# Performance work log

Hardware: AMD Instinct MI355X
Metric: run time of the kernel (lower is better)

Reference implementation:

```python
import jax, jax.numpy as jnp
import numpy as np

N = 100000; S = 8; V = 10000; DE = 64; DH = 64; H = DH + 6; T = 2; E = 250000
MAXP = 10; SZ = 64; OUT = MAXP * SZ; NPLAIN = 6; NAR = 2


def setup_inputs() -> dict:
    key = jax.random.key(0)
    ks = jax.random.split(key, 20)
    rn = lambda k, sh, s=0.1: jax.random.normal(k, sh, jnp.float32) * s
    return {
        "tokens": jax.random.randint(ks[0], (N, S), 0, V, jnp.int32),
        "type_idx": jax.random.randint(ks[1], (N,), 0, 6, jnp.int32),
        "edge_src": jax.random.randint(ks[2], (T, E), 0, N, jnp.int32),
        "edge_dst": jax.random.randint(ks[3], (T, E), 0, N, jnp.int32),
        "map_entry_idx": 123,
        "embed": rn(ks[4], (V, DE), 0.3),
        "Wi_map": rn(ks[5], (3 * DH, DE)), "Wh_map": rn(ks[6], (3 * DH, DH)),
        "bi_map": jnp.zeros((3 * DH,), jnp.float32), "bh_map": jnp.zeros((3 * DH,), jnp.float32),
        "Wi_mem": rn(ks[7], (3 * DH, DE)), "Wh_mem": rn(ks[8], (3 * DH, DH)),
        "bi_mem": jnp.zeros((3 * DH,), jnp.float32), "bh_mem": jnp.zeros((3 * DH,), jnp.float32),
        "Wm_plain": rn(ks[9], (NPLAIN, T, H, H)), "bm_plain": jnp.zeros((NPLAIN, T, H), jnp.float32),
        "Wu_plain": rn(ks[10], (NPLAIN, 2 * H, H)), "bu_plain": jnp.zeros((NPLAIN, H), jnp.float32),
        "Wm_ar": rn(ks[11], (NAR, T, 2 * H, 2 * H)), "bm_ar": jnp.zeros((NAR, T, 2 * H), jnp.float32),
        "Wu_ar": rn(ks[12], (NAR, 4 * H, H)), "bu_ar": jnp.zeros((NAR, H), jnp.float32),
        "W1": rn(ks[13], (H, H)), "b1": jnp.zeros((H,), jnp.float32),
        "W2": rn(ks[14], (H, OUT)), "b2": jnp.zeros((OUT,), jnp.float32),
    }


def _gru_last(x_seq, Wi, Wh, bi, bh):
    # x_seq: [S, N, DE] -> last hidden [N, DH] (torch nn.GRU cell math)
    def step(h, x):
        gi = x @ Wi.T + bi
        gh = h @ Wh.T + bh
        ir, iz, inn = jnp.split(gi, 3, axis=-1)
        hr, hz, hn = jnp.split(gh, 3, axis=-1)
        r = jax.nn.sigmoid(ir + hr)
        z = jax.nn.sigmoid(iz + hz)
        n = jnp.tanh(inn + r * hn)
        return (1.0 - z) * n + z * h, None
    h0 = jnp.zeros((x_seq.shape[1], Wh.shape[1]), x_seq.dtype)
    h, _ = jax.lax.scan(step, h0, x_seq)
    return h


def _mp(h, src, dst, Wm, bm, Wu, bu, msg_act, dense_act):
    # per-edge-type linear message on sender state, scatter-max aggregation, dense update
    m = jnp.einsum('ted,tdm->tem', h[src], Wm) + bm[:, None, :]  # [T, E, M]
    if msg_act is not None:
        m = msg_act(m)
    agg = jax.ops.segment_max(m.reshape(-1, m.shape[-1]), dst.reshape(-1), num_segments=h.shape[0])
    agg = jnp.where(jnp.isneginf(agg), 0.0, agg)  # nodes with no incoming edges -> 0
    u = jnp.concatenate([h, agg], axis=-1) @ Wu + bu
    return dense_act(u) if dense_act is not None else u


def _forward(tokens, type_idx, edge_src, edge_dst, map_entry_idx, embed,
             Wi_map, Wh_map, bi_map, bh_map, Wi_mem, Wh_mem, bi_mem, bh_mem,
             Wm_plain, bm_plain, Wu_plain, bu_plain, Wm_ar, bm_ar, Wu_ar, bu_ar,
             W1, b1, W2, b2):
    x_seq = embed[tokens].transpose(1, 0, 2)  # [S, N, DE]
    h_map = _gru_last(x_seq, Wi_map, Wh_map, bi_map, bh_map)
    h_mem = _gru_last(x_seq, Wi_mem, Wh_mem, bi_mem, bh_mem)
    is_map = (type_idx == 0)[:, None]
    is_mem = (type_idx == 5)[:, None]
    node_h = jnp.where(is_map, h_map, jnp.where(is_mem, h_mem, 0.0))
    h = jnp.concatenate([jax.nn.one_hot(type_idx, 6, dtype=node_h.dtype), node_h], axis=-1)  # [N, H]
    li = 0
    for blk in range(2):  # two concat-residual blocks from create_mlp_mp_layers
        saved = h
        for _ in range(3):  # plain MLP MP layers: no msg/dense activation
            h = _mp(h, edge_src, edge_dst, Wm_plain[li], bm_plain[li], Wu_plain[li], bu_plain[li], None, None)
            li += 1
        h = jnp.concatenate([saved, h], axis=-1)  # ConcatResidualLayer -> [N, 2H]
        h = _mp(h, edge_src, edge_dst, Wm_ar[blk], bm_ar[blk], Wu_ar[blk], bu_ar[blk], jax.nn.gelu, jnp.tanh)
    x = h[map_entry_idx]            # select map entry node
    x = jax.nn.relu(x @ W1 + b1)    # trans_layers[0]
    return x @ W2 + b2


def reference(tokens, type_idx, edge_src, edge_dst, map_entry_idx, embed,
              Wi_map, Wh_map, bi_map, bh_map, Wi_mem, Wh_mem, bi_mem, bh_mem,
              Wm_plain, bm_plain, Wu_plain, bu_plain, Wm_ar, bm_ar, Wu_ar, bu_ar,
              W1, b1, W2, b2):
    return _forward(tokens, type_idx, edge_src, edge_dst, map_entry_idx, embed,
                    Wi_map, Wh_map, bi_map, bh_map, Wi_mem, Wh_mem, bi_mem, bh_mem,
                    Wm_plain, bm_plain, Wu_plain, bu_plain, Wm_ar, bm_ar, Wu_ar, bu_ar,
                    W1, b1, W2, b2)
```

## Files before the change

### kernel.cpp

```cpp
#include <hip/hip_runtime.h>
#include <math.h>

#define CAPT 20480
#define R2   (2*CAPT)
#define GLD  136
#define GRR  32

typedef __attribute__((ext_vector_type(8))) short short8;
typedef __attribute__((ext_vector_type(4))) float f32x4;

__device__ __forceinline__ float fexp2_(float x){ return __builtin_amdgcn_exp2f(x); }
__device__ __forceinline__ float frcp_(float x){ return __builtin_amdgcn_rcpf(x); }
__device__ __forceinline__ float ftanh_(float x){
  float t = fexp2_(2.885390082f * x);
  return __builtin_fmaf(-2.f, frcp_(1.f + t), 1.f);
}
__device__ __forceinline__ float fsig_(float x){
  return frcp_(1.f + fexp2_(-1.442695041f * x));
}
__device__ __forceinline__ float fgelu_(float x){
  float x2 = x*x;
  float u  = x * __builtin_fmaf(x2, 0.044715f, 1.0f);
  float e  = fexp2_(u * -2.30220818f);
  return x * frcp_(1.f + e);
}
__device__ __forceinline__ unsigned short f2bf(float x){
  unsigned int u = __float_as_uint(x);
  return (unsigned short)((u + 0x7FFFu + ((u>>16)&1u)) >> 16);
}
__device__ __forceinline__ float bf2f(unsigned short v){
  return __uint_as_float(((unsigned int)v) << 16);
}
__device__ __forceinline__ unsigned int cvt_pk_bf16(float a, float b){
  unsigned int r;
  asm("v_cvt_pk_bf16_f32 %0, %1, %2" : "=v"(r) : "v"(a), "v"(b));
  return r;
}

__global__ void k_prepB(const float* __restrict__ Wm_plain, const float* __restrict__ Wu_plain,
                        const float* __restrict__ Wm_ar, const float* __restrict__ Wu_ar,
                        const float* __restrict__ Wi_map, const float* __restrict__ Wh_map,
                        const float* __restrict__ Wi_mem, const float* __restrict__ Wh_mem,
                        unsigned short* __restrict__ BtArena){
  int id = blockIdx.y;
  int Kp, elems, off;
  if (id < 6){ Kp=96;  elems=15360; off=id*15360; }
  else if (id < 12){ Kp=160; elems=12800; off=92160+(id-6)*12800; }
  else if (id < 14){ Kp=160; elems=51200; off=168960+(id-12)*51200; }
  else if (id < 16){ Kp=320; elems=25600; off=271360+(id-14)*25600; }
  else { Kp=128; elems=32768; off=322560+(id-16)*32768; }
  for (int g = blockIdx.x*256 + threadIdx.x; g < elems; g += 8*256){
    int c = g / Kp, k = g - c*Kp;
    float val = 0.f;
    if (id < 6){
      int li = id; int t = (c >= 80); int cc = c - t*80;
      if (cc < 70 && k < 70) val = Wm_plain[((li*2+t)*70 + k)*70 + cc];
    } else if (id < 12){
      int li = id-6;
      int kk = (k < 70) ? k : ((k >= 80 && k < 150) ? 70 + (k-80) : -1);
      if (c < 70 && kk >= 0) val = Wu_plain[(li*140 + kk)*70 + c];
    } else if (id < 14){
      int blk = id-12; int t = (c >= 160); int cc = c - t*160;
      int kk = (k < 70) ? k : ((k >= 80 && k < 150) ? 70 + (k-80) : -1);
      if (cc < 140 && kk >= 0) val = Wm_ar[(((blk*2+t)*140) + kk)*140 + cc];
    } else if (id < 16){
      int blk = id-14;
      int kk = (k < 70) ? k : ((k >= 80 && k < 150) ? 70 + (k-80)
               : ((k >= 160 && k < 300) ? 140 + (k-160) : -1));
      if (c < 70 && kk >= 0) val = Wu_ar[(blk*280 + kk)*70 + c];
    } else {
      int typ = id-16;
      const float* Wi = typ ? Wi_mem : Wi_map;
      const float* Wh = typ ? Wh_mem : Wh_map;
      if (c < 192) val = (k < 64) ? Wi[c*64 + k] : Wh[c*64 + (k-64)];
      else { int cc = c-192; val = (k >= 64) ? Wh[(128+cc)*64 + (k-64)] : 0.f; }
    }
    BtArena[off + g] = f2bf(val);
  }
}

__global__ void k_prepBias(const float* __restrict__ bm_plain, const float* __restrict__ bu_plain,
                           const float* __restrict__ bm_ar, const float* __restrict__ bu_ar,
                           const float* __restrict__ bi_map, const float* __restrict__ bh_map,
                           const float* __restrict__ bi_mem, const float* __restrict__ bh_mem,
                           float* __restrict__ biasA){
  for (int g = threadIdx.x; g < 2752; g += 256){
    float val = 0.f;
    if (g < 960){ int li=g/160, c=g%160; int t=(c>=80); int cc=c-t*80;
      if (cc<70) val = bm_plain[(li*2+t)*70 + cc]; }
    else if (g < 1440){ int u=g-960; int li=u/80, c=u%80; if (c<70) val = bu_plain[li*70+c]; }
    else if (g < 2080){ int u=g-1440; int blk=u/320, c=u%320; int t=(c>=160); int cc=c-t*160;
      if (cc<140) val = bm_ar[(blk*2+t)*140 + cc]; }
    else if (g < 2240){ int u=g-2080; int blk=u/80, c=u%80; if (c<70) val = bu_ar[blk*70+c]; }
    else { int u=g-2240; int typ=u/256, c=u%256;
      const float* bi = typ ? bi_mem : bi_map; const float* bh = typ ? bh_mem : bh_map;
      val = (c < 192) ? (bi[c]+bh[c]) : bh[128 + (c-192)]; }
    biasA[g] = val;
  }
}

__global__ void k_prepEmb(const float* __restrict__ embed, unsigned short* __restrict__ embB,
                          int total){
  int g = blockIdx.x*256 + threadIdx.x;
  if (g < total) embB[g] = f2bf(embed[g]);
}

__global__ void k_init_h(const int* __restrict__ type_idx, unsigned short* __restrict__ h, int N){
  int g = blockIdx.x*256 + threadIdx.x;
  if (g >= N*80) return;
  int n = g / 80, c = g - n*80;
  h[g] = (c < 6 && type_idx[n] == c) ? (unsigned short)0x3F80 : (unsigned short)0;
}

__global__ void k_compact(const int* __restrict__ type_idx, int* __restrict__ idxcat,
                          int* __restrict__ cnt, int N){
  int n = blockIdx.x*256 + threadIdx.x;
  if (n >= N) return;
  int t = type_idx[n];
  if (t == 0){ int p = atomicAdd(&cnt[0],1); if (p < CAPT) idxcat[p] = n; }
  else if (t == 5){ int p = atomicAdd(&cnt[1],1); if (p < CAPT) idxcat[CAPT+p] = n; }
}

__global__ void k_count(const int* __restrict__ edst, int* __restrict__ deg, int TE){
  int i = blockIdx.x*256 + threadIdx.x;
  if (i < TE) atomicAdd(&deg[edst[i]], 1);
}
__global__ void k_scan1(const int* __restrict__ deg, int* __restrict__ off,
                        int* __restrict__ bsum, int N){
  __shared__ int sh[256];
  int t = threadIdx.x; int base = blockIdx.x*2048;
  int v[8]; int s = 0;
  for (int i=0;i<8;i++){
    int g = base + t*8 + i;
    int x = (g<N)? (((deg[g]+3)>>2)<<2) : 0;
    v[i]=x; s+=x;
  }
  sh[t]=s; __syncthreads();
  for (int o=1;o<256;o<<=1){ int x = (t>=o)? sh[t-o]:0; __syncthreads(); sh[t]+=x; __syncthreads(); }
  if (t==255) bsum[blockIdx.x] = sh[255];
  int run = sh[t]-s;
  for (int i=0;i<8;i++){ int g = base + t*8 + i; if (g<N) off[g]=run; run+=v[i]; }
}
__global__ void k_scan2(int* bsum, int nb){
  if (threadIdx.x==0 && blockIdx.x==0){
    int run=0;
    for(int b=0;b<nb;b++){ int x=bsum[b]; bsum[b]=run; run+=x; }
    bsum[nb]=run;
  }
}
__global__ void k_scan3(int* __restrict__ off, const int* __restrict__ bsum, int N, int nb){
  int g = blockIdx.x*256+threadIdx.x;
  if (g < N) off[g] += bsum[g>>11];
  if (g == 0) off[N] = bsum[nb];
}
__global__ void k_fill(const int* __restrict__ esrc, const int* __restrict__ edst,
                       const int* __restrict__ off, int* __restrict__ cur,
                       int* __restrict__ edata, int TE, int E){
  int i = blockIdx.x*256 + threadIdx.x;
  if (i >= TE) return;
  int d = edst[i];
  int pos = off[d] + atomicAdd(&cur[d], 1);
  edata[pos] = (esrc[i] << 1) | (i >= E ? 1 : 0);
}
__global__ void k_pad(const int* __restrict__ off, const int* __restrict__ cur,
                      int* __restrict__ edata, int N){
  int n = blockIdx.x*256 + threadIdx.x;
  if (n >= N) return;
  int d = cur[n];
  if (d == 0) return;
  int d4 = ((d+3)>>2)<<2;
  int base = off[n];
  int first = edata[base];
  for (int i = d; i < d4; i++) edata[base+i] = first;
}

__global__ __launch_bounds__(256) void kgru(
    const int* __restrict__ idxcat, const int* __restrict__ tokens,
    const unsigned short* __restrict__ embB,
    const unsigned short* __restrict__ Bt, const unsigned short* __restrict__ Bt2,
    const float* __restrict__ bias, const float* __restrict__ bias2,
    unsigned short* __restrict__ hOut)
{
  __shared__ __align__(16) unsigned short As[2][GRR*GLD];
  __shared__ int tokS[GRR*8];
  __shared__ int idxS[GRR];
  int rb = blockIdx.y * CAPT + blockIdx.x * GRR;
  if (idxcat[rb] < 0) return;
  int t = threadIdx.x;
  int lane = t & 63, m = lane & 15, q = lane >> 4, w = t >> 6;
  const unsigned short* Bsel = blockIdx.y ? Bt2 : Bt;
  const float* bsel = blockIdx.y ? bias2 : bias;
  short8 breg[4][4]; float bv[4];
  #pragma unroll
  for (int j=0;j<4;j++){
    int col = (w + 4*j)*16 + m;
    bv[j] = bsel[col];
    #pragma unroll
    for (int kt=0;kt<4;kt++)
      breg[j][kt] = *(const short8*)&Bsel[(size_t)col*128 + kt*32 + q*8];
  }
  if (t < GRR) idxS[t] = idxcat[rb + t];
  if (t < GRR*8){
    int nd = idxcat[rb + (t>>3)]; if (nd < 0) nd = 0;
    tokS[t] = tokens[nd*8 + (t & 7)];
  }
  __syncthreads();
  if (t < GRR*8){
    int row = t >> 3, ch = t & 7;
    *(uint4*)&As[0][row*GLD + ch*8] = *(const uint4*)&embB[(size_t)tokS[row*8]*64 + ch*8];
  }
  for (int j = t; j < GRR*32; j += 256){
    int row = j >> 5, k2 = (j & 31)*2;
    *(unsigned int*)&As[0][row*GLD + 64 + k2] = 0;
  }
  __syncthreads();
  unsigned short hreg[2][4];
  #pragma unroll
  for (int rt=0;rt<2;rt++)
    #pragma unroll
    for (int i=0;i<4;i++) hreg[rt][i] = 0;
  int u = w*16 + m;
  int p = 0;
  for (int s = 0; s < 8; s++){
    uint4 xr;
    if (s < 7 && t < GRR*8){
      int row = t >> 3, ch = t & 7;
      xr = *(const uint4*)&embB[(size_t)tokS[row*8 + s + 1]*64 + ch*8];
    }
    f32x4 acc[2][4] = {};
    #pragma unroll
    for (int kt=0;kt<4;kt++){
      short8 af[2];
      #pragma unroll
      for (int rt=0;rt<2;rt++)
        af[rt] = *(const short8*)&As[p][(rt*16+m)*GLD + kt*32 + q*8];
      #pragma unroll
      for (int j=0;j<4;j++)
        #pragma unroll
        for (int rt=0;rt<2;rt++)
          acc[rt][j] = __builtin_amdgcn_mfma_f32_16x16x32_bf16(af[rt], breg[j][kt], acc[rt][j], 0,0,0);
    }
    #pragma unroll
    for (int rt=0;rt<2;rt++){
      float hv[4];
      #pragma unroll
      for (int i=0;i<4;i++){
        float xrg = acc[rt][0][i] + bv[0];
        float xzg = acc[rt][1][i] + bv[1];
        float xng = acc[rt][2][i] + bv[2];
        float hng = acc[rt][3][i] + bv[3];
        float pm = frcp_(1.f + fexp2_(1.442695041f*xrg));
        float zz = frcp_(1.f + fexp2_(-1.442695041f*xzg));
        float a  = __builtin_fmaf(-pm, hng, xng);
        float th = ftanh_(a);
        float hp = bf2f(hreg[rt][i]);
        hv[i] = __builtin_fmaf(zz, hp - th, th);
      }
      unsigned int plo = cvt_pk_bf16(hv[0], hv[1]);
      unsigned int phi = cvt_pk_bf16(hv[2], hv[3]);
      hreg[rt][0] = (unsigned short)plo;
      hreg[rt][1] = (unsigned short)(plo >> 16);
      hreg[rt][2] = (unsigned short)phi;
      hreg[rt][3] = (unsigned short)(phi >> 16);
    }
    if (s < 7){
      #pragma unroll
      for (int rt=0;rt<2;rt++)
        #pragma unroll
        for (int i=0;i<4;i++)
          As[p^1][(rt*16 + q*4 + i)*GLD + 64 + u] = hreg[rt][i];
      if (t < GRR*8){
        int row = t >> 3, ch = t & 7;
        *(uint4*)&As[p^1][row*GLD + ch*8] = xr;
      }
      __syncthreads();
      p ^= 1;
    } else {
      #pragma unroll
      for (int rt=0;rt<2;rt++)
        #pragma unroll
        for (int i=0;i<4;i++){
          int nd = idxS[rt*16 + q*4 + i];
          if (nd >= 0) hOut[(size_t)nd*80 + 6 + u] = hreg[rt][i];
        }
    }
  }
}

template<int RTR, int KT, int CT, int ACT>
__global__ __launch_bounds__(256) void wgemm(
    const unsigned short* __restrict__ A0, int w0, int ldA0,
    const unsigned short* __restrict__ A1, int w1, int ldA1,
    const unsigned short* __restrict__ A2, int w2, int ldA2,
    const unsigned short* __restrict__ Bt, int KpB,
    const float* __restrict__ bias,
    unsigned short* __restrict__ C, int ldC,
    int rows, int tiles)
{
  constexpr int Kpad = KT*32;
  constexpr int NRT  = RTR/16;
  constexpr int CPT  = (RTR*Kpad/8)/256;
  __shared__ __align__(16) unsigned short As[RTR*Kpad];
  int t = threadIdx.x;
  int lane = t & 63, m = lane & 15, q = lane >> 4, w = t >> 6;
  int tileBase = blockIdx.y * (4*CT);
  int rtEnd = (rows + RTR - 1)/RTR;
  int tr = blockIdx.x;
  if (tr >= rtEnd) return;

  short8 breg[CT][KT]; float bv[CT]; bool val[CT]; int colr[CT];
  #pragma unroll
  for (int j=0;j<CT;j++){
    int tt = tileBase + w + 4*j;
    val[j] = (tt < tiles);
    int col = tt*16 + m;
    colr[j] = col;
    bv[j] = 0.f;
    if (val[j]){
      bv[j] = bias[col];
      #pragma unroll
      for (int kt=0;kt<KT;kt++)
        breg[j][kt] = *(const short8*)&Bt[(size_t)col*KpB + kt*32 + q*8];
    } else {
      #pragma unroll
      for (int kt=0;kt<KT;kt++) breg[j][kt] = (short8){0,0,0,0,0,0,0,0};
    }
  }

  int w01 = w0 + w1, w012 = w0 + w1 + w2;
  uint4 r[CPT];
  #pragma unroll
  for (int i=0;i<CPT;i++){
    int c = i*256 + t;
    int row = c / (KT*4), kc = (c - row*(KT*4))*8;
    int gr = tr*RTR + row;
    uint4 v = {0,0,0,0};
    if (gr < rows && kc < w012){
      const unsigned short* sp;
      if (kc < w0)       sp = A0 + (size_t)gr*ldA0 + kc;
      else if (kc < w01) sp = A1 + (size_t)gr*ldA1 + (kc - w0);
      else               sp = A2 + (size_t)gr*ldA2 + (kc - w01);
      v = *(const uint4*)sp;
    }
    r[i] = v;
  }
  #pragma unroll
  for (int i=0;i<CPT;i++){
    int c = i*256 + t;
    int row = c / (KT*4), ch = c - row*(KT*4);
    int phys = ch ^ (row & 3);
    *(uint4*)&As[row*Kpad + phys*8] = r[i];
  }
  __syncthreads();

  f32x4 acc[NRT][CT] = {};
  #pragma unroll
  for (int kt=0;kt<KT;kt++){
    short8 af[NRT];
    #pragma unroll
    for (int rt=0;rt<NRT;rt++)
      af[rt] = *(const short8*)&As[(rt*16+m)*Kpad + (((kt*4+q) ^ (m&3))*8)];
    #pragma unroll
    for (int j=0;j<CT;j++)
      #pragma unroll
      for (int rt=0;rt<NRT;rt++)
        acc[rt][j] = __builtin_amdgcn_mfma_f32_16x16x32_bf16(af[rt], breg[j][kt], acc[rt][j], 0,0,0);
  }
  bool tfull = (tr*RTR + RTR <= rows);
#define EPILOG(CHK)                                                         \
    _Pragma("unroll")                                                       \
    for (int rt=0;rt<NRT;rt++){                                             \
      int rbase = tr*RTR + rt*16 + q*4;                                     \
      _Pragma("unroll")                                                     \
      for (int j=0;j<CT;j++){                                               \
        if (!val[j]) continue;                                              \
        float v0 = acc[rt][j][0] + bv[j];                                   \
        float v1 = acc[rt][j][1] + bv[j];                                   \
        float v2 = acc[rt][j][2] + bv[j];                                   \
        float v3 = acc[rt][j][3] + bv[j];                                   \
        if (ACT == 1){ v0=fgelu_(v0); v1=fgelu_(v1); v2=fgelu_(v2); v3=fgelu_(v3); } \
        else if (ACT == 2){ v0=ftanh_(v0); v1=ftanh_(v1); v2=ftanh_(v2); v3=ftanh_(v3); } \
        unsigned int plo = cvt_pk_bf16(v0, v1);                             \
        unsigned int phi = cvt_pk_bf16(v2, v3);                             \
        size_t cb = (size_t)rbase*ldC + colr[j];                            \
        if (!CHK || rbase+0 < rows) C[cb]           = (unsigned short)plo;         \
        if (!CHK || rbase+1 < rows) C[cb + ldC]     = (unsigned short)(plo >> 16); \
        if (!CHK || rbase+2 < rows) C[cb + 2*ldC]   = (unsigned short)phi;         \
        if (!CHK || rbase+3 < rows) C[cb + 3*ldC]   = (unsigned short)(phi >> 16); \
      }                                                                     \
    }
  if (tfull){ EPILOG(false) } else { EPILOG(true) }
#undef EPILOG
}

__global__ __launch_bounds__(256) void k_aggregate(
    const int* __restrict__ off, const int* __restrict__ edata,
    const unsigned short* __restrict__ P2, int ldP, int off1,
    unsigned short* __restrict__ agg, int M, int N, int WPN)
{
  int t = threadIdx.x;
  int lane = t & 63, w = t >> 6;
  int nbase, c;
  if (WPN == 1){
    nbase = blockIdx.x*16 + w*4;
    c = 2*lane;
  } else {
    nbase = blockIdx.x*8 + (w>>1)*4;
    c = (w & 1)*80 + 2*lane;
  }
  nbase = __builtin_amdgcn_readfirstlane(nbase);
  if (nbase >= N) return;
  bool act = (lane < 40);
  const float NEG = -__builtin_inff();
  int e[4], e1[4];
  float f0[4], f1[4];
  #pragma unroll
  for (int j=0;j<4;j++){
    int n = nbase + j;
    bool v = (n < N);
    e[j]  = v ? __builtin_amdgcn_readfirstlane(off[n])     : 0;
    e1[j] = v ? __builtin_amdgcn_readfirstlane(off[n + 1]) : 0;
    f0[j] = NEG; f1[j] = NEG;
  }
  for (;;){
    bool cond[4];
    bool any = false;
    #pragma unroll
    for (int j=0;j<4;j++){ cond[j] = (e[j] < e1[j]); any |= cond[j]; }
    if (!any) break;
    unsigned int rr[4][4];
    #pragma unroll
    for (int j=0;j<4;j++){
      if (cond[j]){
        int4 g = *(const int4*)&edata[e[j]];
        int b0 = (g.x>>1)*ldP + (g.x&1)*off1;
        int b1 = (g.y>>1)*ldP + (g.y&1)*off1;
        int b2 = (g.z>>1)*ldP + (g.z&1)*off1;
        int b3 = (g.w>>1)*ldP + (g.w&1)*off1;
        if (act){
          rr[j][0] = *(const unsigned int*)(P2 + b0 + c);
          rr[j][1] = *(const unsigned int*)(P2 + b1 + c);
          rr[j][2] = *(const unsigned int*)(P2 + b2 + c);
          rr[j][3] = *(const unsigned int*)(P2 + b3 + c);
        }
      }
    }
    #pragma unroll
    for (int j=0;j<4;j++){
      if (cond[j]){
        if (act){
          unsigned int u0 = rr[j][0], u1 = rr[j][1], u2 = rr[j][2], u3 = rr[j][3];
          f0[j] = fmaxf(f0[j], fmaxf(fmaxf(__uint_as_float(u0<<16), __uint_as_float(u1<<16)),
                                     fmaxf(__uint_as_float(u2<<16), __uint_as_float(u3<<16))));
          f1[j] = fmaxf(f1[j], fmaxf(fmaxf(__uint_as_float(u0&0xFFFF0000u), __uint_as_float(u1&0xFFFF0000u)),
                                     fmaxf(__uint_as_float(u2&0xFFFF0000u), __uint_as_float(u3&0xFFFF0000u))));
        }
        e[j] += 4;
      }
    }
  }
  if (act){
    #pragma unroll
    for (int j=0;j<4;j++){
      int n = nbase + j;
      if (n >= N) continue;
      unsigned int o = (__float_as_uint(f0[j] == NEG ? 0.f : f0[j]) >> 16)
                     |  (__float_as_uint(f1[j] == NEG ? 0.f : f1[j]) & 0xFFFF0000u);
      *(unsigned int*)(agg + (size_t)n*M + c) = o;
    }
  }
}

__global__ void k_head(const unsigned short* __restrict__ h, const int* __restrict__ entry,
                       const float* __restrict__ W1, const float* __restrict__ b1,
                       const float* __restrict__ W2, const float* __restrict__ b2,
                       float* __restrict__ out){
  __shared__ float x[70], x1[70];
  int t = threadIdx.x;
  if (t < 70) x[t] = bf2f(h[(size_t)(*entry)*80 + t]);
  __syncthreads();
  if (t < 70){
    float s = b1[t];
    for (int i=0;i<70;i++) s += x[i]*W1[i*70 + t];
    x1[t] = fmaxf(s, 0.f);
  }
  __syncthreads();
  if (t < 640){
    float s = b2[t];
    for (int i=0;i<70;i++) s += x1[i]*W2[i*640 + t];
    out[t] = s;
  }
}

extern "C" void kernel_launch(void* const* d_in, const int* in_sizes, int n_in,
                              void* d_out, int out_size, void* d_ws, size_t ws_size,
                              hipStream_t stream) {
  const int*   tokens   = (const int*)d_in[0];
  const int*   type_idx = (const int*)d_in[1];
  const int*   esrc     = (const int*)d_in[2];
  const int*   edst     = (const int*)d_in[3];
  const int*   entry    = (const int*)d_in[4];
  const float* embed    = (const float*)d_in[5];
  const float* Wi_map   = (const float*)d_in[6];
  const float* Wh_map   = (const float*)d_in[7];
  const float* bi_map   = (const float*)d_in[8];
  const float* bh_map   = (const float*)d_in[9];
  const float* Wi_mem   = (const float*)d_in[10];
  const float* Wh_mem   = (const float*)d_in[11];
  const float* bi_mem   = (const float*)d_in[12];
  const float* bh_mem   = (const float*)d_in[13];
  const float* Wm_plain = (const float*)d_in[14];
  const float* bm_plain = (const float*)d_in[15];
  const float* Wu_plain = (const float*)d_in[16];
  const float* bu_plain = (const float*)d_in[17];
  const float* Wm_ar    = (const float*)d_in[18];
  const float* bm_ar    = (const float*)d_in[19];
  const float* Wu_ar    = (const float*)d_in[20];
  const float* bu_ar    = (const float*)d_in[21];
  const float* W1 = (const float*)d_in[22];
  const float* b1 = (const float*)d_in[23];
  const float* W2 = (const float*)d_in[24];
  const float* b2 = (const float*)d_in[25];
  float* out = (float*)d_out;

  const int N  = in_sizes[1];
  const int TE = in_sizes[2];
  const int E  = TE / 2;
  const int V64 = in_sizes[5];

  char* p = (char*)d_ws;
  auto alloc = [&](size_t bytes)->char* { char* r = p; p += (bytes + 255) & ~(size_t)255; return r; };
  unsigned short* hA  = (unsigned short*)alloc((size_t)N*80*2);
  unsigned short* hB  = (unsigned short*)alloc((size_t)N*80*2);
  unsigned short* hC  = (unsigned short*)alloc((size_t)N*80*2);
  unsigned short* P2  = (unsigned short*)alloc((size_t)N*320*2);
  unsigned short* agg = (unsigned short*)alloc((size_t)N*160*2);
  int* deg    = (int*)alloc((size_t)N*4);
  int* curp   = (int*)alloc((size_t)N*4);
  int* off    = (int*)alloc((size_t)(N+8)*4);
  int* edata  = (int*)alloc((size_t)(TE + 4*N + 16)*4);
  int* sbsum  = (int*)alloc(256*4);
  int* cnt    = (int*)alloc(16*4);
  int* idxcat = (int*)alloc((size_t)R2*4);
  unsigned short* BtA  = (unsigned short*)alloc(388096*2);
  float* biasA = (float*)alloc(2752*4);
  unsigned short* embB = (unsigned short*)alloc((size_t)V64*2);

  hipMemsetAsync(idxcat, 0xFF, (size_t)R2*4, stream);
  hipMemsetAsync(cnt,    0,    16*4, stream);
  hipMemsetAsync(deg,    0,    (size_t)N*4, stream);
  hipMemsetAsync(curp,   0,    (size_t)N*4, stream);

  k_prepB<<<dim3(8,18), 256, 0, stream>>>(Wm_plain, Wu_plain, Wm_ar, Wu_ar,
                                          Wi_map, Wh_map, Wi_mem, Wh_mem, BtA);
  k_prepBias<<<1, 256, 0, stream>>>(bm_plain, bu_plain, bm_ar, bu_ar,
                                    bi_map, bh_map, bi_mem, bh_mem, biasA);
  k_prepEmb<<<(V64+255)/256, 256, 0, stream>>>(embed, embB, V64);
  k_init_h<<<(N*80+255)/256, 256, 0, stream>>>(type_idx, hA, N);
  k_compact<<<(N+255)/256, 256, 0, stream>>>(type_idx, idxcat, cnt, N);

  k_count<<<(TE+255)/256, 256, 0, stream>>>(edst, deg, TE);
  int nb = (N + 2047)/2048;
  k_scan1<<<nb, 256, 0, stream>>>(deg, off, sbsum, N);
  k_scan2<<<1, 64, 0, stream>>>(sbsum, nb);
  k_scan3<<<(N+255)/256, 256, 0, stream>>>(off, sbsum, N, nb);
  k_fill<<<(TE+255)/256, 256, 0, stream>>>(esrc, edst, off, curp, edata, TE, E);
  k_pad<<<(N+255)/256, 256, 0, stream>>>(off, curp, edata, N);

  kgru<<<dim3(CAPT/GRR, 2), 256, 0, stream>>>(
      idxcat, tokens, embB,
      BtA + 322560, BtA + 322560 + 32768,
      biasA + 2240, biasA + 2240 + 256, hA);

  const int T64 = (N + 63)/64;
  const int T32 = (N + 31)/32;

  unsigned short* cur = hA; unsigned short* f1 = hB; unsigned short* f2 = hC;
  int li = 0;
  for (int blk = 0; blk < 2; blk++){
    unsigned short* saved = cur;
    unsigned short* ins[3]  = {cur, f1, f2};
    unsigned short* outs[3] = {f1, f2, f1};
    for (int j = 0; j < 3; j++){
      unsigned short* X = ins[j]; unsigned short* Yo = outs[j];
      wgemm<64,3,3,0><<<dim3(T64,1), 256, 0, stream>>>(
          X, 80, 80,  nullptr, 0, 0,  nullptr, 0, 0,
          BtA + li*15360, 96, biasA + li*160,
          P2, 160, N, 10);
      k_aggregate<<<(N+15)/16, 256, 0, stream>>>(off, edata, P2, 160, 80, agg, 80, N, 1);
      wgemm<64,5,2,0><<<dim3(T64,1), 256, 0, stream>>>(
          X, 80, 80,  agg, 80, 80,  nullptr, 0, 0,
          BtA + 92160 + li*12800, 160, biasA + 960 + li*80,
          Yo, 80, N, 5);
      li++;
    }
    wgemm<64,5,3,1><<<dim3(T64,2), 256, 0, stream>>>(
        saved, 80, 80,  f1, 80, 80,  nullptr, 0, 0,
        BtA + 168960 + blk*51200, 160, biasA + 1440 + blk*320,
        P2, 320, N, 20);
    k_aggregate<<<(N+7)/8, 256, 0, stream>>>(off, edata, P2, 320, 160, agg, 160, N, 2);
    wgemm<32,10,2,2><<<dim3(T32,1), 256, 0, stream>>>(
        saved, 80, 80,  f1, 80, 80,  agg, 160, 160,
        BtA + 271360 + blk*25600, 320, biasA + 2080 + blk*80,
        f2, 80, N, 5);
    unsigned short* t3 = cur; cur = f2; f2 = t3;
  }

  k_head<<<1, 640, 0, stream>>>(cur, entry, W1, b1, W2, b2, out);
}
```

Baseline: 779.2 us.

## Make wgemm persistent with double-buffered direct global-to-LDS A-tile loads

The GEMM kernel becomes persistent: a fixed grid (1024 or 512x2 blocks) loops over row tiles, keeps the weight fragments in registers across tiles, and prefetches the next A tile into a second LDS buffer while the current one is multiplied. A-tile loads now use global_load_lds, which writes 16 bytes straight into LDS without passing through VGPRs. The XOR swizzle moves to the source-address side, and padding columns are zeroed once up front. This aims to hide global load latency and cut per-block setup, at the cost of doubled LDS use per block and fewer concurrently resident blocks.

Measured after the change: 770.4 us. About the same (-1.1%).

```diff
diff --git a/kernel.cpp b/kernel.cpp
--- a/kernel.cpp
+++ b/kernel.cpp
@@ -35,6 +35,10 @@
   unsigned int r;
   asm("v_cvt_pk_bf16_f32 %0, %1, %2" : "=v"(r) : "v"(a), "v"(b));
   return r;
+}
+__device__ __forceinline__ void gload_lds16(const unsigned short* g, unsigned short* l){
+  __builtin_amdgcn_global_load_lds((const __attribute__((address_space(1))) void*)g,
+                                   (__attribute__((address_space(3))) void*)l, 16, 0, 0);
 }
 
 __global__ void k_prepB(const float* __restrict__ Wm_plain, const float* __restrict__ Wu_plain,
@@ -299,8 +303,9 @@
 {
   constexpr int Kpad = KT*32;
   constexpr int NRT  = RTR/16;
-  constexpr int CPT  = (RTR*Kpad/8)/256;
-  __shared__ __align__(16) unsigned short As[RTR*Kpad];
+  constexpr int NCH  = KT*4;
+  constexpr int CPT  = (RTR*NCH)/256;
+  __shared__ __align__(16) unsigned short As[2][RTR*Kpad];
   int t = threadIdx.x;
   int lane = t & 63, m = lane & 15, q = lane >> 4, w = t >> 6;
   int tileBase = blockIdx.y * (4*CT);
@@ -328,45 +333,57 @@
   }
 
   int w01 = w0 + w1, w012 = w0 + w1 + w2;
-  uint4 r[CPT];
-  #pragma unroll
-  for (int i=0;i<CPT;i++){
-    int c = i*256 + t;
-    int row = c / (KT*4), kc = (c - row*(KT*4))*8;
-    int gr = tr*RTR + row;
-    uint4 v = {0,0,0,0};
-    if (gr < rows && kc < w012){
-      const unsigned short* sp;
-      if (kc < w0)       sp = A0 + (size_t)gr*ldA0 + kc;
-      else if (kc < w01) sp = A1 + (size_t)gr*ldA1 + (kc - w0);
-      else               sp = A2 + (size_t)gr*ldA2 + (kc - w01);
-      v = *(const uint4*)sp;
-    }
-    r[i] = v;
-  }
-  #pragma unroll
-  for (int i=0;i<CPT;i++){
-    int c = i*256 + t;
-    int row = c / (KT*4), ch = c - row*(KT*4);
-    int phys = ch ^ (row & 3);
-    *(uint4*)&As[row*Kpad + phys*8] = r[i];
-  }
+
+  if (w012 < NCH*8){
+    const uint4 z = {0,0,0,0};
+    for (int c = t; c < RTR*NCH; c += 256){
+      int row = c / NCH, chp = c - row*NCH;
+      if (((chp ^ (row & 3))*8) >= w012){
+        *(uint4*)&As[0][c*8] = z;
+        *(uint4*)&As[1][c*8] = z;
+      }
+    }
+  }
+
+  auto stage = [&](int p, int trr){
+    #pragma unroll
+    for (int i=0;i<CPT;i++){
+      int c = i*256 + t;
+      int row = c / NCH, chp = c - row*NCH;
+      int kc = (chp ^ (row & 3))*8;
+      int gr = trr*RTR + row;
+      unsigned short* ldst = &As[p][(size_t)(i*256 + (t & ~63))*8];
+      if (gr < rows && kc < w012){
+        const unsigned short* sp;
+        if (kc < w0)       sp = A0 + (size_t)gr*ldA0 + kc;
+        else if (kc < w01) sp = A1 + (size_t)gr*ldA1 + (kc - w0);
+        else               sp = A2 + (size_t)gr*ldA2 + (kc - w01);
+        gload_lds16(sp, ldst);
+      }
+    }
+  };
+
+  stage(0, tr);
   __syncthreads();
-
-  f32x4 acc[NRT][CT] = {};
-  #pragma unroll
-  for (int kt=0;kt<KT;kt++){
-    short8 af[NRT];
-    #pragma unroll
-    for (int rt=0;rt<NRT;rt++)
-      af[rt] = *(const short8*)&As[(rt*16+m)*Kpad + (((kt*4+q) ^ (m&3))*8)];
-    #pragma unroll
-    for (int j=0;j<CT;j++)
+  int p = 0;
+  for (;;){
+    int nxt = tr + gridDim.x;
+    bool hasNext = (nxt < rtEnd);
+    if (hasNext) stage(p^1, nxt);
+    f32x4 acc[NRT][CT] = {};
+    #pragma unroll
+    for (int kt=0;kt<KT;kt++){
+      short8 af[NRT];
       #pragma unroll
       for (int rt=0;rt<NRT;rt++)
-        acc[rt][j] = __builtin_amdgcn_mfma_f32_16x16x32_bf16(af[rt], breg[j][kt], acc[rt][j], 0,0,0);
-  }
-  bool tfull = (tr*RTR + RTR <= rows);
+        af[rt] = *(const short8*)&As[p][(rt*16+m)*Kpad + (((kt*4+q) ^ (m&3))*8)];
+      #pragma unroll
+      for (int j=0;j<CT;j++)
+        #pragma unroll
+        for (int rt=0;rt<NRT;rt++)
+          acc[rt][j] = __builtin_amdgcn_mfma_f32_16x16x32_bf16(af[rt], breg[j][kt], acc[rt][j], 0,0,0);
+    }
+    bool tfull = (tr*RTR + RTR <= rows);
 #define EPILOG(CHK)                                                         \
     _Pragma("unroll")                                                       \
     for (int rt=0;rt<NRT;rt++){                                             \
@@ -389,8 +406,12 @@
         if (!CHK || rbase+3 < rows) C[cb + 3*ldC]   = (unsigned short)(phi >> 16); \
       }                                                                     \
     }
-  if (tfull){ EPILOG(false) } else { EPILOG(true) }
+    if (tfull){ EPILOG(false) } else { EPILOG(true) }
 #undef EPILOG
+    if (!hasNext) break;
+    __syncthreads();
+    p ^= 1; tr = nxt;
+  }
 }
 
 __global__ __launch_bounds__(256) void k_aggregate(
@@ -572,9 +593,6 @@
       BtA + 322560, BtA + 322560 + 32768,
       biasA + 2240, biasA + 2240 + 256, hA);
 
-  const int T64 = (N + 63)/64;
-  const int T32 = (N + 31)/32;
-
   unsigned short* cur = hA; unsigned short* f1 = hB; unsigned short* f2 = hC;
   int li = 0;
   for (int blk = 0; blk < 2; blk++){
@@ -583,23 +601,23 @@
     unsigned short* outs[3] = {f1, f2, f1};
     for (int j = 0; j < 3; j++){
       unsigned short* X = ins[j]; unsigned short* Yo = outs[j];
-      wgemm<64,3,3,0><<<dim3(T64,1), 256, 0, stream>>>(
+      wgemm<64,3,3,0><<<dim3(1024,1), 256, 0, stream>>>(
           X, 80, 80,  nullptr, 0, 0,  nullptr, 0, 0,
           BtA + li*15360, 96, biasA + li*160,
           P2, 160, N, 10);
       k_aggregate<<<(N+15)/16, 256, 0, stream>>>(off, edata, P2, 160, 80, agg, 80, N, 1);
-      wgemm<64,5,2,0><<<dim3(T64,1), 256, 0, stream>>>(
+      wgemm<64,5,2,0><<<dim3(1024,1), 256, 0, stream>>>(
           X, 80, 80,  agg, 80, 80,  nullptr, 0, 0,
           BtA + 92160 + li*12800, 160, biasA + 960 + li*80,
           Yo, 80, N, 5);
       li++;
     }
-    wgemm<64,5,3,1><<<dim3(T64,2), 256, 0, stream>>>(
+    wgemm<64,5,3,1><<<dim3(512,2), 256, 0, stream>>>(
         saved, 80, 80,  f1, 80, 80,  nullptr, 0, 0,
         BtA + 168960 + blk*51200, 160, biasA + 1440 + blk*320,
         P2, 320, N, 20);
     k_aggregate<<<(N+7)/8, 256, 0, stream>>>(off, edata, P2, 320, 160, agg, 160, N, 2);
-    wgemm<32,10,2,2><<<dim3(T32,1), 256, 0, stream>>>(
+    wgemm<32,10,2,2><<<dim3(1024,1), 256, 0, stream>>>(
         saved, 80, 80,  f1, 80, 80,  agg, 160, 160,
         BtA + 271360 + blk*25600, 320, biasA + 2080 + blk*80,
         f2, 80, N, 5);
```
